# Optimization experiments

Hardware: AMD Instinct MI355X
Metric: run time of the kernel (lower is better)

## Reference

```python
import jax, jax.numpy as jnp
import numpy as np
from jax import lax

N = 7  # patch size


def _conv3d(x, w, b):
    # x: [B,1,D,H,W], w: [1,1,3,3,3], b: [1]; VALID conv, stride 1
    y = lax.conv_general_dilated(x, w, (1, 1, 1), 'VALID',
                                 dimension_numbers=('NCDHW', 'OIDHW', 'NCDHW'))
    return y + b.reshape(1, -1, 1, 1, 1)


def _patches(x, k):
    # x: [B,1,D,H,W] -> [B*D'*H'*W', 1, k, k, k], row-major (kd,kh,kw) like torch unfold
    p = lax.conv_general_dilated_patches(x, (k, k, k), (1, 1, 1), 'VALID')
    # p: [B, k^3, D', H', W'] -> [B, D', H', W', k^3]
    p = jnp.transpose(p, (0, 2, 3, 4, 1))
    return p.reshape(-1, 1, k, k, k)


def setup_inputs() -> dict:
    key = jax.random.key(0)
    ks = jax.random.split(key, 12)
    inp = {
        'x': jax.random.normal(ks[0], (1, 1, 32, 128, 128), dtype=jnp.float32),
        'domain_neighbor': jax.random.uniform(ks[1], (1, 1, 9, 9, 9), dtype=jnp.float32),
        'guide_im': jax.random.normal(ks[2], (1, 1, 32, 128, 128), dtype=jnp.float32),
        # range coefficient conv stack (2 layers of Conv3d(1,1,3))
        'rw0': jax.random.normal(ks[3], (1, 1, 3, 3, 3), dtype=jnp.float32) * 0.3,
        'rb0': jnp.full((1,), 0.1, dtype=jnp.float32),
        'rw1': jax.random.normal(ks[4], (1, 1, 3, 3, 3), dtype=jnp.float32) * 0.3,
        'rb1': jnp.full((1,), 0.1, dtype=jnp.float32),
        # domain coefficient conv stack
        'dw0': jax.random.normal(ks[5], (1, 1, 3, 3, 3), dtype=jnp.float32) * 0.3,
        'db0': jnp.full((1,), 0.1, dtype=jnp.float32),
        'dw1': jax.random.normal(ks[6], (1, 1, 3, 3, 3), dtype=jnp.float32) * 0.3,
        'db1': jnp.full((1,), 0.1, dtype=jnp.float32),
    }
    return inp


def reference(x, domain_neighbor, guide_im, rw0, rb0, rw1, rb1, dw0, db0, dw1, db1):
    n = N
    c = n // 2
    # ---- range kernel: per-patch |guide - center|, then tiny conv stack ----
    g = _patches(guide_im, n)                     # [P,1,n,n,n]
    g = jnp.abs(g - g[:, :, c, c, c][:, :, None, None, None])
    rk = jax.nn.relu(_conv3d(g, rw0, rb0))
    rk = jax.nn.relu(_conv3d(rk, rw1, rb1))       # [P,1,3,3,3]
    # ---- domain kernel: center crop of distance kernel, same conv stack ----
    M = domain_neighbor.shape[2]
    cx = M // 2 - c
    dn = domain_neighbor[:, :, cx:cx + n, cx:cx + n, cx:cx + n]  # [1,1,n,n,n]
    dk = jax.nn.relu(_conv3d(dn, dw0, db0))
    dk = jax.nn.relu(_conv3d(dk, dw1, db1))       # [1,1,3,3,3]
    weights = dk * rk + 1e-10                     # [P,1,3,3,3]
    # ---- weighted average over 3x3x3 neighborhood of truncated x ----
    p = (n - 3) // 2
    xt = x[:, :, p:x.shape[2] - p, p:x.shape[3] - p, p:x.shape[4] - p]
    xu = _patches(xt, 3)                          # [P,1,3,3,3]
    num = jnp.sum(xu * weights, axis=(2, 3, 4))   # [P,1]
    den = jnp.sum(weights, axis=(2, 3, 4))        # [P,1]
    out = num / den
    B = x.shape[0]
    return out.reshape(B, 1, x.shape[2] - n + 1, x.shape[3] - n + 1, x.shape[4] - n + 1)
```

## Files before the change

kernel.cpp:

```cpp
#include <hip/hip_runtime.h>

#define OD 26
#define OH 122
#define OW 122
#define GS (128*128)
#define NOUT (OD*OH*OW)

__global__ void compute_dk_kernel(const float* __restrict__ dn,
                                  const float* __restrict__ dw0, const float* __restrict__ db0,
                                  const float* __restrict__ dw1, const float* __restrict__ db1,
                                  float* __restrict__ dk_out) {
    __shared__ float d0[125];
    int t = threadIdx.x;
    if (t < 125) {
        int tz = t / 25, ty = (t / 5) % 5, tx = t % 5;
        float acc = db0[0];
        #pragma unroll
        for (int kz = 0; kz < 3; ++kz)
            #pragma unroll
            for (int ky = 0; ky < 3; ++ky)
                #pragma unroll
                for (int kx = 0; kx < 3; ++kx)
                    acc += dw0[kz*9 + ky*3 + kx] *
                           dn[(1+tz+kz)*81 + (1+ty+ky)*9 + (1+tx+kx)];
        d0[t] = fmaxf(acc, 0.0f);
    }
    __syncthreads();
    if (t < 27) {
        int rz = t / 9, ry = (t / 3) % 3, rx = t % 3;
        float acc = db1[0];
        #pragma unroll
        for (int kz = 0; kz < 3; ++kz)
            #pragma unroll
            for (int ky = 0; ky < 3; ++ky)
                #pragma unroll
                for (int kx = 0; kx < 3; ++kx)
                    acc += dw1[kz*9 + ky*3 + kx] * d0[(rz+kz)*25 + (ry+ky)*5 + (rx+kx)];
        dk_out[t] = fmaxf(acc, 0.0f);
    }
}

__global__ __launch_bounds__(256) void jbf_main_kernel(
        const float* __restrict__ x, const float* __restrict__ guide,
        const float* __restrict__ rw0p, const float* __restrict__ rb0p,
        const float* __restrict__ rw1p, const float* __restrict__ rb1p,
        const float* __restrict__ dkp, float* __restrict__ out) {
    int idx = blockIdx.x * blockDim.x + threadIdx.x;
    if (idx >= NOUT) return;
    int x0 = idx % OW;
    int y0 = (idx / OW) % OH;
    int z0 = idx / (OW * OH);

    float rw0[27], rw1[27], dkv[27];
    #pragma unroll
    for (int i = 0; i < 27; ++i) { rw0[i] = rw0p[i]; rw1[i] = rw1p[i]; dkv[i] = dkp[i]; }
    const float rb0 = rb0p[0], rb1 = rb1p[0];

    const float gc = guide[(z0+3)*GS + (y0+3)*128 + (x0+3)];

    float t0[125];
    #pragma unroll
    for (int i = 0; i < 125; ++i) t0[i] = rb0;

    #pragma unroll
    for (int gz = 0; gz < 7; ++gz) {
        float a[49];
        const float* gp = guide + (z0+gz)*GS + y0*128 + x0;
        #pragma unroll
        for (int gy = 0; gy < 7; ++gy)
            #pragma unroll
            for (int gx = 0; gx < 7; ++gx)
                a[gy*7 + gx] = fabsf(gp[gy*128 + gx] - gc);
        #pragma unroll
        for (int kz = 0; kz < 3; ++kz) {
            const int tz = gz - kz;
            if (tz < 0 || tz > 4) continue;
            #pragma unroll
            for (int ty = 0; ty < 5; ++ty)
                #pragma unroll
                for (int ky = 0; ky < 3; ++ky)
                    #pragma unroll
                    for (int tx = 0; tx < 5; ++tx)
                        #pragma unroll
                        for (int kx = 0; kx < 3; ++kx)
                            t0[tz*25 + ty*5 + tx] +=
                                rw0[kz*9 + ky*3 + kx] * a[(ty+ky)*7 + (tx+kx)];
        }
    }
    #pragma unroll
    for (int i = 0; i < 125; ++i) t0[i] = fmaxf(t0[i], 0.0f);

    float num = 0.0f, den = 0.0f;
    #pragma unroll
    for (int rz = 0; rz < 3; ++rz)
        #pragma unroll
        for (int ry = 0; ry < 3; ++ry)
            #pragma unroll
            for (int rx = 0; rx < 3; ++rx) {
                float acc = rb1;
                #pragma unroll
                for (int kz = 0; kz < 3; ++kz)
                    #pragma unroll
                    for (int ky = 0; ky < 3; ++ky)
                        #pragma unroll
                        for (int kx = 0; kx < 3; ++kx)
                            acc += rw1[kz*9 + ky*3 + kx] *
                                   t0[(rz+kz)*25 + (ry+ky)*5 + (rx+kx)];
                const float w = dkv[rz*9 + ry*3 + rx] * fmaxf(acc, 0.0f) + 1e-10f;
                den += w;
                num += w * x[(z0+2+rz)*GS + (y0+2+ry)*128 + (x0+2+rx)];
            }

    out[idx] = num / den;
}

extern "C" void kernel_launch(void* const* d_in, const int* in_sizes, int n_in,
                              void* d_out, int out_size, void* d_ws, size_t ws_size,
                              hipStream_t stream) {
    const float* x     = (const float*)d_in[0];
    const float* dn    = (const float*)d_in[1];
    const float* guide = (const float*)d_in[2];
    const float* rw0   = (const float*)d_in[3];
    const float* rb0   = (const float*)d_in[4];
    const float* rw1   = (const float*)d_in[5];
    const float* rb1   = (const float*)d_in[6];
    const float* dw0   = (const float*)d_in[7];
    const float* db0   = (const float*)d_in[8];
    const float* dw1   = (const float*)d_in[9];
    const float* db1   = (const float*)d_in[10];
    float* out = (float*)d_out;
    float* dk  = (float*)d_ws;

    compute_dk_kernel<<<1, 128, 0, stream>>>(dn, dw0, db0, dw1, db1, dk);

    int nblk = (NOUT + 255) / 256;
    jbf_main_kernel<<<nblk, 256, 0, stream>>>(x, guide, rw0, rb0, rw1, rb1, dk, out);
}
```

Baseline: 169.1 us.

## Stream first conv through rolling 3-slice buffer and fuse second conv incrementally

Replaces the 125-float intermediate with a rolling 3-slice ring buffer and row-wise guide loads, accumulating the second 3x3x3 conv into 27 accumulators as each first-layer slice completes. This cuts live registers so more waves fit per CU and avoids spilling. Block size drops to 64 threads with launch bounds (64,4), and dk weights are read directly from global memory instead of being cached in registers. Because the ring-buffer slot indices depend on unrolled loop constants, full unrolling is needed to keep them in registers.

```diff
diff --git a/kernel.cpp b/kernel.cpp
--- a/kernel.cpp
+++ b/kernel.cpp
@@ -40,77 +40,100 @@
     }
 }
 
-__global__ __launch_bounds__(256) void jbf_main_kernel(
+__global__ __launch_bounds__(64, 4) void jbf_main_kernel(
         const float* __restrict__ x, const float* __restrict__ guide,
         const float* __restrict__ rw0p, const float* __restrict__ rb0p,
         const float* __restrict__ rw1p, const float* __restrict__ rb1p,
         const float* __restrict__ dkp, float* __restrict__ out) {
-    int idx = blockIdx.x * blockDim.x + threadIdx.x;
+    int idx = blockIdx.x * 64 + threadIdx.x;
     if (idx >= NOUT) return;
     int x0 = idx % OW;
     int y0 = (idx / OW) % OH;
     int z0 = idx / (OW * OH);
 
-    float rw0[27], rw1[27], dkv[27];
+    float rw0[27], rw1[27];
     #pragma unroll
-    for (int i = 0; i < 27; ++i) { rw0[i] = rw0p[i]; rw1[i] = rw1p[i]; dkv[i] = dkp[i]; }
+    for (int i = 0; i < 27; ++i) { rw0[i] = rw0p[i]; rw1[i] = rw1p[i]; }
     const float rb0 = rb0p[0], rb1 = rb1p[0];
 
-    const float gc = guide[(z0+3)*GS + (y0+3)*128 + (x0+3)];
+    const float* gbase = guide + z0*GS + y0*128 + x0;
+    const float gc = gbase[3*GS + 3*128 + 3];
 
-    float t0[125];
+    float t0[3][25];
+    float acc[27];
     #pragma unroll
-    for (int i = 0; i < 125; ++i) t0[i] = rb0;
+    for (int i = 0; i < 27; ++i) acc[i] = rb1;
 
     #pragma unroll
     for (int gz = 0; gz < 7; ++gz) {
-        float a[49];
-        const float* gp = guide + (z0+gz)*GS + y0*128 + x0;
+        if (gz <= 4) {
+            const int sl = gz % 3;
+            #pragma unroll
+            for (int i = 0; i < 25; ++i) t0[sl][i] = rb0;
+        }
+        const float* gp = gbase + gz*GS;
         #pragma unroll
-        for (int gy = 0; gy < 7; ++gy)
+        for (int gy = 0; gy < 7; ++gy) {
+            float s[7];
             #pragma unroll
-            for (int gx = 0; gx < 7; ++gx)
-                a[gy*7 + gx] = fabsf(gp[gy*128 + gx] - gc);
-        #pragma unroll
-        for (int kz = 0; kz < 3; ++kz) {
-            const int tz = gz - kz;
-            if (tz < 0 || tz > 4) continue;
+            for (int j = 0; j < 7; ++j) s[j] = gp[gy*128 + j] - gc;
             #pragma unroll
-            for (int ty = 0; ty < 5; ++ty)
+            for (int kz = 0; kz < 3; ++kz) {
+                const int tz = gz - kz;
+                if (tz < 0 || tz > 4) continue;
+                const int tsl = tz % 3;
                 #pragma unroll
-                for (int ky = 0; ky < 3; ++ky)
+                for (int ky = 0; ky < 3; ++ky) {
+                    const int ty = gy - ky;
+                    if (ty < 0 || ty > 4) continue;
                     #pragma unroll
                     for (int tx = 0; tx < 5; ++tx)
                         #pragma unroll
                         for (int kx = 0; kx < 3; ++kx)
-                            t0[tz*25 + ty*5 + tx] +=
-                                rw0[kz*9 + ky*3 + kx] * a[(ty+ky)*7 + (tx+kx)];
+                            t0[tsl][ty*5 + tx] =
+                                fmaf(rw0[kz*9 + ky*3 + kx], fabsf(s[tx + kx]),
+                                     t0[tsl][ty*5 + tx]);
+                }
+            }
+        }
+        const int tzc = gz - 2;
+        if (tzc >= 0 && tzc <= 4) {
+            const int csl = tzc % 3;
+            #pragma unroll
+            for (int i = 0; i < 25; ++i) t0[csl][i] = fmaxf(t0[csl][i], 0.0f);
+            #pragma unroll
+            for (int rz = 0; rz < 3; ++rz) {
+                const int kz2 = tzc - rz;
+                if (kz2 < 0 || kz2 > 2) continue;
+                #pragma unroll
+                for (int ry = 0; ry < 3; ++ry)
+                    #pragma unroll
+                    for (int rx = 0; rx < 3; ++rx)
+                        #pragma unroll
+                        for (int ky = 0; ky < 3; ++ky)
+                            #pragma unroll
+                            for (int kx = 0; kx < 3; ++kx)
+                                acc[rz*9 + ry*3 + rx] =
+                                    fmaf(rw1[kz2*9 + ky*3 + kx],
+                                         t0[csl][(ry+ky)*5 + (rx+kx)],
+                                         acc[rz*9 + ry*3 + rx]);
+            }
         }
     }
-    #pragma unroll
-    for (int i = 0; i < 125; ++i) t0[i] = fmaxf(t0[i], 0.0f);
 
     float num = 0.0f, den = 0.0f;
+    const float* xb = x + (z0+2)*GS + (y0+2)*128 + (x0+2);
     #pragma unroll
     for (int rz = 0; rz < 3; ++rz)
         #pragma unroll
         for (int ry = 0; ry < 3; ++ry)
             #pragma unroll
             for (int rx = 0; rx < 3; ++rx) {
-                float acc = rb1;
-                #pragma unroll
-                for (int kz = 0; kz < 3; ++kz)
-                    #pragma unroll
-                    for (int ky = 0; ky < 3; ++ky)
-                        #pragma unroll
-                        for (int kx = 0; kx < 3; ++kx)
-                            acc += rw1[kz*9 + ky*3 + kx] *
-                                   t0[(rz+kz)*25 + (ry+ky)*5 + (rx+kx)];
-                const float w = dkv[rz*9 + ry*3 + rx] * fmaxf(acc, 0.0f) + 1e-10f;
+                const float w = dkp[rz*9 + ry*3 + rx] * fmaxf(acc[rz*9 + ry*3 + rx], 0.0f)
+                                + 1e-10f;
                 den += w;
-                num += w * x[(z0+2+rz)*GS + (y0+2+ry)*128 + (x0+2+rx)];
+                num = fmaf(w, xb[rz*GS + ry*128 + rx], num);
             }
-
     out[idx] = num / den;
 }
 
@@ -133,6 +156,6 @@
 
     compute_dk_kernel<<<1, 128, 0, stream>>>(dn, dw0, db0, dw1, db1, dk);
 
-    int nblk = (NOUT + 255) / 256;
-    jbf_main_kernel<<<nblk, 256, 0, stream>>>(x, guide, rw0, rb0, rw1, rb1, dk, out);
+    int nblk = (NOUT + 63) / 64;
+    jbf_main_kernel<<<nblk, 64, 0, stream>>>(x, guide, rw0, rb0, rw1, rb1, dk, out);
 }
```

Result: slower. 490.3 us (+189.9%).

## Tile guide image into shared memory with 3D blocks and stream rows

Applied to the files above, without the earlier changes.

Each block now covers an 8x8x4 output tile on a 3D grid and first loads the 14x14x10 guide halo into shared memory, so the 7x7x7 patch reads come from LDS instead of repeated global loads. The inner loop now works one guide row at a time, keeping a 7-element row in registers instead of a 49-element slice, which lowers register pressure. It also uses explicit fma and reads the domain kernel values directly from global memory. In exchange it adds a block-wide barrier, about 7.8 KB of shared memory per block, and some idle threads in edge tiles.

```diff
diff --git a/kernel.cpp b/kernel.cpp
--- a/kernel.cpp
+++ b/kernel.cpp
@@ -5,6 +5,12 @@
 #define OW 122
 #define GS (128*128)
 #define NOUT (OD*OH*OW)
+
+#define TLX 14
+#define TLY 14
+#define TLZ 10
+#define TLSLICE (TLX*TLY)
+#define TLN (TLSLICE*TLZ)
 
 __global__ void compute_dk_kernel(const float* __restrict__ dn,
                                   const float* __restrict__ dw0, const float* __restrict__ db0,
@@ -45,18 +51,38 @@
         const float* __restrict__ rw0p, const float* __restrict__ rb0p,
         const float* __restrict__ rw1p, const float* __restrict__ rb1p,
         const float* __restrict__ dkp, float* __restrict__ out) {
-    int idx = blockIdx.x * blockDim.x + threadIdx.x;
-    if (idx >= NOUT) return;
-    int x0 = idx % OW;
-    int y0 = (idx / OW) % OH;
-    int z0 = idx / (OW * OH);
+    __shared__ float gl[TLN];
 
-    float rw0[27], rw1[27], dkv[27];
+    const int xb = blockIdx.x * 8;
+    const int yb = blockIdx.y * 8;
+    const int zb = blockIdx.z * 4;
+
+    for (int i = threadIdx.x; i < TLN; i += 256) {
+        const int gx = i % TLX;
+        const int gy = (i / TLX) % TLY;
+        const int gz = i / TLSLICE;
+        const int sx = min(xb + gx, 127);
+        const int sy = min(yb + gy, 127);
+        const int sz = min(zb + gz, 31);
+        gl[i] = guide[sz*GS + sy*128 + sx];
+    }
+    __syncthreads();
+
+    const int tx = threadIdx.x & 7;
+    const int ty = (threadIdx.x >> 3) & 7;
+    const int tz = threadIdx.x >> 6;
+    const int x0 = xb + tx;
+    const int y0 = yb + ty;
+    const int z0 = zb + tz;
+    if (x0 >= OW || y0 >= OH || z0 >= OD) return;
+
+    float rw0[27], rw1[27];
     #pragma unroll
-    for (int i = 0; i < 27; ++i) { rw0[i] = rw0p[i]; rw1[i] = rw1p[i]; dkv[i] = dkp[i]; }
+    for (int i = 0; i < 27; ++i) { rw0[i] = rw0p[i]; rw1[i] = rw1p[i]; }
     const float rb0 = rb0p[0], rb1 = rb1p[0];
 
-    const float gc = guide[(z0+3)*GS + (y0+3)*128 + (x0+3)];
+    const float* glb = &gl[tz*TLSLICE + ty*TLX + tx];
+    const float gc = glb[3*TLSLICE + 3*TLX + 3];
 
     float t0[125];
     #pragma unroll
@@ -64,33 +90,36 @@
 
     #pragma unroll
     for (int gz = 0; gz < 7; ++gz) {
-        float a[49];
-        const float* gp = guide + (z0+gz)*GS + y0*128 + x0;
         #pragma unroll
-        for (int gy = 0; gy < 7; ++gy)
+        for (int gy = 0; gy < 7; ++gy) {
+            float s[7];
             #pragma unroll
-            for (int gx = 0; gx < 7; ++gx)
-                a[gy*7 + gx] = fabsf(gp[gy*128 + gx] - gc);
-        #pragma unroll
-        for (int kz = 0; kz < 3; ++kz) {
-            const int tz = gz - kz;
-            if (tz < 0 || tz > 4) continue;
+            for (int j = 0; j < 7; ++j)
+                s[j] = glb[gz*TLSLICE + gy*TLX + j] - gc;
             #pragma unroll
-            for (int ty = 0; ty < 5; ++ty)
+            for (int kz = 0; kz < 3; ++kz) {
+                const int tz1 = gz - kz;
+                if (tz1 < 0 || tz1 > 4) continue;
                 #pragma unroll
-                for (int ky = 0; ky < 3; ++ky)
+                for (int ky = 0; ky < 3; ++ky) {
+                    const int ty1 = gy - ky;
+                    if (ty1 < 0 || ty1 > 4) continue;
                     #pragma unroll
-                    for (int tx = 0; tx < 5; ++tx)
+                    for (int txx = 0; txx < 5; ++txx)
                         #pragma unroll
                         for (int kx = 0; kx < 3; ++kx)
-                            t0[tz*25 + ty*5 + tx] +=
-                                rw0[kz*9 + ky*3 + kx] * a[(ty+ky)*7 + (tx+kx)];
+                            t0[tz1*25 + ty1*5 + txx] =
+                                fmaf(rw0[kz*9 + ky*3 + kx], fabsf(s[txx + kx]),
+                                     t0[tz1*25 + ty1*5 + txx]);
+                }
+            }
         }
     }
     #pragma unroll
     for (int i = 0; i < 125; ++i) t0[i] = fmaxf(t0[i], 0.0f);
 
     float num = 0.0f, den = 0.0f;
+    const float* xbp = x + (z0+2)*GS + (y0+2)*128 + (x0+2);
     #pragma unroll
     for (int rz = 0; rz < 3; ++rz)
         #pragma unroll
@@ -104,14 +133,14 @@
                     for (int ky = 0; ky < 3; ++ky)
                         #pragma unroll
                         for (int kx = 0; kx < 3; ++kx)
-                            acc += rw1[kz*9 + ky*3 + kx] *
-                                   t0[(rz+kz)*25 + (ry+ky)*5 + (rx+kx)];
-                const float w = dkv[rz*9 + ry*3 + rx] * fmaxf(acc, 0.0f) + 1e-10f;
+                            acc = fmaf(rw1[kz*9 + ky*3 + kx],
+                                       t0[(rz+kz)*25 + (ry+ky)*5 + (rx+kx)], acc);
+                const float w = dkp[rz*9 + ry*3 + rx] * fmaxf(acc, 0.0f) + 1e-10f;
                 den += w;
-                num += w * x[(z0+2+rz)*GS + (y0+2+ry)*128 + (x0+2+rx)];
+                num = fmaf(w, xbp[rz*GS + ry*128 + rx], num);
             }
 
-    out[idx] = num / den;
+    out[(z0*OH + y0)*OW + x0] = num / den;
 }
 
 extern "C" void kernel_launch(void* const* d_in, const int* in_sizes, int n_in,
@@ -133,6 +162,6 @@
 
     compute_dk_kernel<<<1, 128, 0, stream>>>(dn, dw0, db0, dw1, db1, dk);
 
-    int nblk = (NOUT + 255) / 256;
-    jbf_main_kernel<<<nblk, 256, 0, stream>>>(x, guide, rw0, rb0, rw1, rb1, dk, out);
+    dim3 grid((OW + 7) / 8, (OH + 7) / 8, (OD + 3) / 4);
+    jbf_main_kernel<<<grid, 256, 0, stream>>>(x, guide, rw0, rb0, rw1, rb1, dk, out);
 }
```

Result: faster. 147.5 us (-12.8%).
